# Kernel tuning notes

Hardware: AMD Instinct MI355X
Metric: run time of the kernel (lower is better)

## Reference

```python
import jax, jax.numpy as jnp
import numpy as np

N_DR, N_P, N_DIS = 8000, 20000, 5000
N_MF, N_BP, N_CC, N_PATH = 3000, 8000, 2000, 2392
H, B = 128, 65536
F_FINGER, F_SEQ, F_DIS = 1024, 400, 512
EPS = 1e-5


def _gcn(e, xs, ndst, W, b):
    # DGL GraphConv(norm='none', in==out): sum-aggregate src feats, then linear, then ReLU
    agg = jax.ops.segment_sum(xs[e[0]], e[1], num_segments=ndst)
    return jax.nn.relu(agg @ W + b)


def _sage(e, xs, xd, Wp, bp, Ws, Wn, b):
    # DGL SAGEConv(aggregator_type='pool'): max over relu(fc_pool(src)) + fc_self(dst), then ReLU
    h = jax.nn.relu(xs @ Wp + bp)
    agg = jax.ops.segment_max(h[e[0]], e[1], num_segments=xd.shape[0])
    agg = jnp.where(jnp.isfinite(agg), agg, 0.0)  # zero-in-degree dst -> 0 (DGL convention)
    return jax.nn.relu(xd @ Ws + agg @ Wn + b)


def _bn_relu(x, g, b):
    # BatchNorm1d in training mode (batch stats, biased var) + ReLU
    m = x.mean(0)
    v = x.var(0)
    return jax.nn.relu(g * (x - m) * jax.lax.rsqrt(v + EPS) + b)


def setup_inputs():
    key = jax.random.key(0)
    ks = iter(jax.random.split(key, 80))
    def nrm(shape, s=0.05):
        return jax.random.normal(next(ks), shape, dtype=jnp.float32) * s
    def edges(E, ns, nd):
        k1, k2 = jax.random.split(next(ks))
        return jnp.stack([jax.random.randint(k1, (E,), 0, ns, dtype=jnp.int32),
                          jax.random.randint(k2, (E,), 0, nd, dtype=jnp.int32)])
    inp = {}
    inp["x_dr"] = jax.random.randint(next(ks), (B, 1), 0, N_DR, dtype=jnp.int32)
    inp["x_p"] = jax.random.randint(next(ks), (B, 1), 0, N_P, dtype=jnp.int32)
    inp["finger_feats"] = nrm((N_DR, F_FINGER), 1.0)
    inp["seq_feats"] = nrm((N_P, F_SEQ), 1.0)
    inp["disease_feat"] = nrm((N_DIS, F_DIS), 1.0)
    inp["MF_feat"] = jnp.eye(N_MF, dtype=jnp.float32)   # identity feats, as in source
    inp["BP_feat"] = jnp.eye(N_BP, dtype=jnp.float32)
    inp["CC_feat"] = jnp.eye(N_CC, dtype=jnp.float32)
    inp["Pathway_feat"] = jnp.eye(N_PATH, dtype=jnp.float32)
    inp["e_dtdr"] = edges(100000, N_DIS, N_DR)
    inp["e_dmdr"] = edges(100000, N_DIS, N_DR)
    inp["e_dp"] = edges(200000, N_DIS, N_P)
    inp["e_drtd"] = edges(100000, N_DR, N_DIS)
    inp["e_drmd"] = edges(100000, N_DR, N_DIS)
    inp["e_pd"] = edges(200000, N_P, N_DIS)
    inp["e_ddi"] = edges(300000, N_DR, N_DR)
    inp["e_ppi"] = edges(600000, N_P, N_P)
    inp["e_mf_sim"] = edges(100000, N_MF, N_MF)
    inp["e_bp_sim"] = edges(300000, N_BP, N_BP)
    inp["e_cc_sim"] = edges(60000, N_CC, N_CC)
    inp["e_mf2p"] = edges(200000, N_MF, N_P)
    inp["e_bp2p"] = edges(400000, N_BP, N_P)
    inp["e_cc2p"] = edges(100000, N_CC, N_P)
    inp["e_path2p"] = edges(100000, N_PATH, N_P)
    inp["W_dr_emb"] = nrm((F_FINGER, H)); inp["b_dr_emb"] = jnp.zeros((H,), jnp.float32)
    inp["W_p_emb"] = nrm((F_SEQ, H)); inp["b_p_emb"] = jnp.zeros((H,), jnp.float32)
    inp["W_d_emb"] = nrm((F_DIS, H)); inp["b_d_emb"] = jnp.zeros((H,), jnp.float32)
    inp["W_mf_emb"] = nrm((N_MF, H)); inp["b_mf_emb"] = jnp.zeros((H,), jnp.float32)
    inp["W_bp_emb"] = nrm((N_BP, H)); inp["b_bp_emb"] = jnp.zeros((H,), jnp.float32)
    inp["W_cc_emb"] = nrm((N_CC, H)); inp["b_cc_emb"] = jnp.zeros((H,), jnp.float32)
    inp["W_path_emb"] = nrm((N_PATH, H)); inp["b_path_emb"] = jnp.zeros((H,), jnp.float32)
    inp["W_gcn"] = nrm((7, H, H)); inp["b_gcn"] = jnp.zeros((7, H), jnp.float32)
    inp["Wp_sage"] = nrm((8, H, H)); inp["bp_sage"] = jnp.zeros((8, H), jnp.float32)
    inp["Ws_sage"] = nrm((8, H, H)); inp["Wn_sage"] = nrm((8, H, H))
    inp["b_sage"] = jnp.zeros((8, H), jnp.float32)
    inp["W1"] = nrm((7 * H, 2 * H)); inp["b1"] = jnp.zeros((2 * H,), jnp.float32)
    inp["g1"] = jnp.ones((2 * H,), jnp.float32); inp["be1"] = jnp.zeros((2 * H,), jnp.float32)
    inp["W2"] = nrm((2 * H, H)); inp["b2"] = jnp.zeros((H,), jnp.float32)
    inp["g2"] = jnp.ones((H,), jnp.float32); inp["be2"] = jnp.zeros((H,), jnp.float32)
    inp["W3"] = nrm((H, 64)); inp["b3"] = jnp.zeros((64,), jnp.float32)
    inp["g3"] = jnp.ones((64,), jnp.float32); inp["be3"] = jnp.zeros((64,), jnp.float32)
    inp["Wo"] = nrm((64, 1)); inp["bo"] = jnp.zeros((1,), jnp.float32)
    return inp


def reference(x_dr, x_p, e_dtdr, e_dmdr, e_dp, e_drtd, e_drmd, e_pd, e_ddi, e_ppi,
              e_mf_sim, e_bp_sim, e_cc_sim, e_mf2p, e_bp2p, e_cc2p, e_path2p,
              finger_feats, seq_feats, disease_feat, MF_feat, BP_feat, CC_feat, Pathway_feat,
              W_dr_emb, b_dr_emb, W_p_emb, b_p_emb, W_d_emb, b_d_emb,
              W_mf_emb, b_mf_emb, W_bp_emb, b_bp_emb, W_cc_emb, b_cc_emb, W_path_emb, b_path_emb,
              W_gcn, b_gcn, Wp_sage, bp_sage, Ws_sage, Wn_sage, b_sage,
              W1, b1, g1, be1, W2, b2, g2, be2, W3, b3, g3, be3, Wo, bo):
    relu = jax.nn.relu
    # node-type input embeddings (Linear + ReLU)
    h_dr0 = relu(finger_feats @ W_dr_emb + b_dr_emb)
    h_p0 = relu(seq_feats @ W_p_emb + b_p_emb)
    h_d = relu(disease_feat @ W_d_emb + b_d_emb)
    h_mf = relu(MF_feat @ W_mf_emb + b_mf_emb)
    h_bp = relu(BP_feat @ W_bp_emb + b_bp_emb)
    h_cc = relu(CC_feat @ W_cc_emb + b_cc_emb)
    h_path = relu(Pathway_feat @ W_path_emb + b_path_emb)
    # GO similarity GCNs with residual
    mf = _gcn(e_mf_sim, h_mf, N_MF, W_gcn[0], b_gcn[0]) + h_mf
    bp = _gcn(e_bp_sim, h_bp, N_BP, W_gcn[1], b_gcn[1]) + h_bp
    cc = _gcn(e_cc_sim, h_cc, N_CC, W_gcn[2], b_gcn[2]) + h_cc
    # GO->protein and pathway->protein (HeteroGraphConv, sum aggregate)
    h_p_go = (_gcn(e_mf2p, mf, N_P, W_gcn[3], b_gcn[3])
              + _gcn(e_bp2p, bp, N_P, W_gcn[4], b_gcn[4])
              + _gcn(e_cc2p, cc, N_P, W_gcn[5], b_gcn[5]))
    h_p_path = _gcn(e_path2p, h_path, N_P, W_gcn[6], b_gcn[6])
    # heterogeneous SAGE layer over my_G (weights shared across the two applications)
    def S(i):
        return (Wp_sage[i], bp_sage[i], Ws_sage[i], Wn_sage[i], b_sage[i])
    def hetero(hdr, hp, hd):
        dr = (_sage(e_dtdr, hd, hdr, *S(0)) + _sage(e_dmdr, hd, hdr, *S(1))
              + _sage(e_ddi, hdr, hdr, *S(6)))
        p = _sage(e_dp, hd, hp, *S(2)) + _sage(e_ppi, hp, hp, *S(7))
        d = (_sage(e_drtd, hdr, hd, *S(3)) + _sage(e_drmd, hdr, hd, *S(4))
             + _sage(e_pd, hp, hd, *S(5)))
        return dr, p, d
    dr1, p1, d1 = hetero(h_dr0, h_p0, h_d)
    dr2, p2, _ = hetero(dr1, p1, d1)
    dr_new = jnp.concatenate([h_dr0, dr1, dr2], axis=1)                 # [N_DR, 3H]
    p_new = jnp.concatenate([h_p0, p1, p2, h_p_go + h_p_path], axis=1)  # [N_P, 4H]
    h = jnp.concatenate([dr_new[x_dr[:, 0]], p_new[x_p[:, 0]]], axis=1)  # [B, 7H]
    h = _bn_relu(h @ W1 + b1, g1, be1)
    h = _bn_relu(h @ W2 + b2, g2, be2)
    h = _bn_relu(h @ W3 + b3, g3, be3)
    return jax.nn.sigmoid(h @ Wo + bo)
```

## Files before the change

kernel.cpp:

```cpp
#include <hip/hip_runtime.h>

#define NCSR 15
#define MAXP 6
#define MAXT 8
#define NPT 21
#define NWT 37

typedef __attribute__((ext_vector_type(8))) short bfrag;
typedef __attribute__((ext_vector_type(4))) float ffrag;

__device__ __forceinline__ float b2f(unsigned short s) {
  return __uint_as_float(((unsigned int)s) << 16);
}
__device__ __forceinline__ unsigned short f2b(float f) {
  unsigned int u = __float_as_uint(f);
  u = (u + 0x7FFFu + ((u >> 16) & 1u)) >> 16;
  return (unsigned short)u;
}
__device__ __forceinline__ float ldf(const void* p, size_t i, int bf) {
  if (bf) return b2f(((const unsigned short*)p)[i]);
  return ((const float*)p)[i];
}
__device__ __forceinline__ int4 ld8(const void* p, size_t i, int bf) {
  if (bf) return *(const int4*)((const unsigned short*)p + i);
  const float* pf = (const float*)p + i;
  float4 f0 = *(const float4*)pf;
  float4 f1 = *(const float4*)(pf + 4);
  int4 v;
  v.x = (int)((unsigned)f2b(f0.x) | ((unsigned)f2b(f0.y) << 16));
  v.y = (int)((unsigned)f2b(f0.z) | ((unsigned)f2b(f0.w) << 16));
  v.z = (int)((unsigned)f2b(f1.x) | ((unsigned)f2b(f1.y) << 16));
  v.w = (int)((unsigned)f2b(f1.z) | ((unsigned)f2b(f1.w) << 16));
  return v;
}

struct CsrDesc {
  const int* src; const int* dst; int E; int n_dst;
  int* rowptr; unsigned short* csrc; int* slot; int pad;
};
struct CsrArgs { CsrDesc d[NCSR]; };

struct PTask { const void* src; float* dst; int n; int pad; };
struct PArgs { PTask t[NPT]; };

struct WTask { const void* src; unsigned short* dst; int K; int N; int eoff; int pad; };
struct WArgs { WTask t[NWT]; };

struct MPass { const unsigned short* A; const unsigned short* W; const float* bias; int lda; int ldw; int flags; };
struct MTask {
  MPass p[MAXP];
  const unsigned short* R; unsigned short* C;
  int npass, n, K, ldc, relu, pad;
};
struct MArgs { MTask t[MAXT]; };

struct GTask { const int* rowptr; const unsigned short* csrc; const unsigned short* X; unsigned short* out; int n_dst; int ldx; int mode; int pad; };
struct GArgs { GTask t[MAXT]; };

struct ETask { const void* A; const unsigned short* W; const float* bias; unsigned short* C; int n, K, ldc, pad; };
struct EArgs { ETask t[3]; };

struct BTask { const void* w; const float* b; unsigned short* out; int n; int pad[3]; };
struct BArgs { BTask t[4]; };

__global__ void k_flag(const unsigned int* probe, int* flag) {
  if (threadIdx.x == 0) *flag = (probe[0] == 0x3F800000u) ? 0 : 1;
}

__global__ void k_cv_params(PArgs args, const int* __restrict__ flagp) {
  const int bf = *flagp;
  const PTask T = args.t[blockIdx.y];
  for (int i = blockIdx.x * blockDim.x + threadIdx.x; i < T.n; i += gridDim.x * blockDim.x)
    T.dst[i] = ldf(T.src, (size_t)i, bf);
}

__global__ void k_cv_wt(WArgs args, const int* __restrict__ flagp) {
  const int bf = *flagp;
  const WTask T = args.t[blockIdx.y];
  const int total = T.K * T.N;
  const size_t eoff = (size_t)T.eoff;
  for (int i = blockIdx.x * blockDim.x + threadIdx.x; i < total; i += gridDim.x * blockDim.x) {
    int n = i / T.K, k = i - n * T.K;
    T.dst[i] = f2b(ldf(T.src, eoff + (size_t)k * T.N + n, bf));
  }
}

__global__ void k_biasrelu_multi(BArgs args, const int* __restrict__ flagp) {
  const int bf = *flagp;
  const BTask T = args.t[blockIdx.y];
  const int n8 = T.n >> 3;
  for (int i = blockIdx.x * blockDim.x + threadIdx.x; i < n8; i += gridDim.x * blockDim.x) {
    int base = i << 3;
    int4 v = ld8(T.w, (size_t)base, bf);
    const unsigned short* pv = (const unsigned short*)&v;
    const int cb = base & 127;
    unsigned short o[8];
#pragma unroll
    for (int j = 0; j < 8; ++j) {
      float f = b2f(pv[j]) + T.b[cb + j];
      o[j] = f2b(f > 0.f ? f : 0.f);
    }
    *(int4*)(T.out + base) = *(const int4*)o;
  }
}

__global__ void k_csr_count(CsrArgs args) {
  const CsrDesc cd = args.d[blockIdx.y];
  for (int e = blockIdx.x * blockDim.x + threadIdx.x; e < cd.E; e += gridDim.x * blockDim.x)
    cd.slot[e] = atomicAdd(&cd.rowptr[cd.dst[e] + 1], 1);
}

__global__ void k_csr_scan(CsrArgs args) {
  const CsrDesc cd = args.d[blockIdx.x];
  const int n = cd.n_dst + 1;
  const int t = threadIdx.x;
  const int lane = t & 63, w = t >> 6;
  __shared__ int wsum[16];
  int carry = 0;
  for (int base = 0; base < n; base += 1024) {
    int i = base + t;
    int v = (i < n) ? cd.rowptr[i] : 0;
    for (int off = 1; off < 64; off <<= 1) {
      int u = __shfl_up(v, off, 64);
      if (lane >= off) v += u;
    }
    if (lane == 63) wsum[w] = v;
    __syncthreads();
    if (w == 0) {
      int s = (lane < 16) ? wsum[lane] : 0;
      for (int off = 1; off < 16; off <<= 1) {
        int u = __shfl_up(s, off, 64);
        if (lane >= off) s += u;
      }
      if (lane < 16) wsum[lane] = s;
    }
    __syncthreads();
    int nv = v + carry + (w > 0 ? wsum[w - 1] : 0);
    if (i < n) cd.rowptr[i] = nv;
    carry += wsum[15];
    __syncthreads();
  }
}

__global__ void k_csr_fill(CsrArgs args) {
  const CsrDesc cd = args.d[blockIdx.y];
  for (int e = blockIdx.x * blockDim.x + threadIdx.x; e < cd.E; e += gridDim.x * blockDim.x) {
    int d = cd.dst[e];
    cd.csrc[cd.rowptr[d] + cd.slot[e]] = (unsigned short)cd.src[e];
  }
}

__global__ void k_gather_multi(GArgs args) {
  const GTask T = args.t[blockIdx.y];
  int w = (blockIdx.x * blockDim.x + threadIdx.x) >> 6;
  if (w >= T.n_dst) return;
  int lane = threadIdx.x & 63;
  int beg = T.rowptr[w], end = T.rowptr[w + 1];
  float a0 = 0.f, a1 = 0.f;
  int j = beg;
  if (T.mode == 0) {
    for (; j + 3 < end; j += 4) {
      unsigned int u0 = ((const unsigned int*)(T.X + (size_t)T.csrc[j] * T.ldx))[lane];
      unsigned int u1 = ((const unsigned int*)(T.X + (size_t)T.csrc[j + 1] * T.ldx))[lane];
      unsigned int u2 = ((const unsigned int*)(T.X + (size_t)T.csrc[j + 2] * T.ldx))[lane];
      unsigned int u3 = ((const unsigned int*)(T.X + (size_t)T.csrc[j + 3] * T.ldx))[lane];
      a0 += __uint_as_float(u0 << 16) + __uint_as_float(u1 << 16)
          + __uint_as_float(u2 << 16) + __uint_as_float(u3 << 16);
      a1 += __uint_as_float(u0 & 0xFFFF0000u) + __uint_as_float(u1 & 0xFFFF0000u)
          + __uint_as_float(u2 & 0xFFFF0000u) + __uint_as_float(u3 & 0xFFFF0000u);
    }
    for (; j < end; ++j) {
      unsigned int u0 = ((const unsigned int*)(T.X + (size_t)T.csrc[j] * T.ldx))[lane];
      a0 += __uint_as_float(u0 << 16);
      a1 += __uint_as_float(u0 & 0xFFFF0000u);
    }
  } else {
    for (; j + 3 < end; j += 4) {
      unsigned int u0 = ((const unsigned int*)(T.X + (size_t)T.csrc[j] * T.ldx))[lane];
      unsigned int u1 = ((const unsigned int*)(T.X + (size_t)T.csrc[j + 1] * T.ldx))[lane];
      unsigned int u2 = ((const unsigned int*)(T.X + (size_t)T.csrc[j + 2] * T.ldx))[lane];
      unsigned int u3 = ((const unsigned int*)(T.X + (size_t)T.csrc[j + 3] * T.ldx))[lane];
      a0 = fmaxf(fmaxf(a0, fmaxf(__uint_as_float(u0 << 16), __uint_as_float(u1 << 16))),
                 fmaxf(__uint_as_float(u2 << 16), __uint_as_float(u3 << 16)));
      a1 = fmaxf(fmaxf(a1, fmaxf(__uint_as_float(u0 & 0xFFFF0000u), __uint_as_float(u1 & 0xFFFF0000u))),
                 fmaxf(__uint_as_float(u2 & 0xFFFF0000u), __uint_as_float(u3 & 0xFFFF0000u)));
    }
    for (; j < end; ++j) {
      unsigned int u0 = ((const unsigned int*)(T.X + (size_t)T.csrc[j] * T.ldx))[lane];
      a0 = fmaxf(a0, __uint_as_float(u0 << 16));
      a1 = fmaxf(a1, __uint_as_float(u0 & 0xFFFF0000u));
    }
  }
  unsigned int* po = (unsigned int*)(T.out + (size_t)w * 128);
  po[lane] = (unsigned int)f2b(a0) | ((unsigned int)f2b(a1) << 16);
}

__launch_bounds__(256)
__global__ void k_mg(MArgs args) {
  const MTask* T = &args.t[blockIdx.y];
  const int n = T->n;
  const int row0 = blockIdx.x * 64;
  if (row0 >= n) return;
  __shared__ __align__(16) unsigned short As[64][72];
  __shared__ __align__(16) unsigned short Ws[128][72];
  const int t = threadIdx.x;
  const int wave = t >> 6, lane = t & 63;
  const int m16 = lane & 15, kq = lane >> 4;
  const int K = T->K;
  ffrag acc[4][2], accO[4][2];
#pragma unroll
  for (int i = 0; i < 4; ++i)
#pragma unroll
    for (int j = 0; j < 2; ++j) { acc[i][j] = (ffrag)0.f; accO[i][j] = (ffrag)0.f; }
  const int colbase = wave * 32;
  for (int ip = 0; ip < T->npass; ++ip) {
    const unsigned short* Ap = T->p[ip].A;
    const unsigned short* Wp = T->p[ip].W;
    const int lda = T->p[ip].lda, ldw = T->p[ip].ldw;
    for (int k0 = 0; k0 < K; k0 += 64) {
      __syncthreads();
#pragma unroll
      for (int e = t; e < 512; e += 256) {
        int r = e >> 3, c = e & 7;
        int row = row0 + r;
        int4 v = {0, 0, 0, 0};
        if (row < n) v = *(const int4*)(Ap + (size_t)row * lda + k0 + c * 8);
        *(int4*)&As[r][c * 8] = v;
      }
#pragma unroll
      for (int e = t; e < 1024; e += 256) {
        int nn = e >> 3, c = e & 7;
        *(int4*)&Ws[nn][c * 8] = *(const int4*)(Wp + (size_t)nn * ldw + k0 + c * 8);
      }
      __syncthreads();
#pragma unroll
      for (int kk = 0; kk < 64; kk += 32) {
        bfrag b0 = *(const bfrag*)&Ws[colbase + m16][kk + kq * 8];
        bfrag b1 = *(const bfrag*)&Ws[colbase + 16 + m16][kk + kq * 8];
#pragma unroll
        for (int rb = 0; rb < 4; ++rb) {
          bfrag a = *(const bfrag*)&As[rb * 16 + m16][kk + kq * 8];
          acc[rb][0] = __builtin_amdgcn_mfma_f32_16x16x32_bf16(a, b0, acc[rb][0], 0, 0, 0);
          acc[rb][1] = __builtin_amdgcn_mfma_f32_16x16x32_bf16(a, b1, acc[rb][1], 0, 0, 0);
        }
      }
    }
    if (T->p[ip].flags & 1) {
      const float* bias = T->p[ip].bias;
      float bv0 = bias ? bias[colbase + m16] : 0.f;
      float bv1 = bias ? bias[colbase + 16 + m16] : 0.f;
#pragma unroll
      for (int rb = 0; rb < 4; ++rb)
#pragma unroll
        for (int cb = 0; cb < 2; ++cb) {
          float bv = cb ? bv1 : bv0;
#pragma unroll
          for (int r = 0; r < 4; ++r) {
            float v = acc[rb][cb][r] + bv;
            if (T->relu) v = v > 0.f ? v : 0.f;
            accO[rb][cb][r] += v;
          }
          acc[rb][cb] = (ffrag)0.f;
        }
    }
  }
  const int ldc = T->ldc;
#pragma unroll
  for (int rb = 0; rb < 4; ++rb)
#pragma unroll
    for (int cb = 0; cb < 2; ++cb) {
      int col = colbase + cb * 16 + m16;
#pragma unroll
      for (int r = 0; r < 4; ++r) {
        int row = row0 + rb * 16 + kq * 4 + r;
        if (row < n) {
          float v = accO[rb][cb][r];
          if (T->R) v += b2f(T->R[(size_t)row * ldc + col]);
          T->C[(size_t)row * ldc + col] = f2b(v);
        }
      }
    }
}

__launch_bounds__(256)
__global__ void k_embed_multi(EArgs args, const int* __restrict__ flagp) {
  const ETask T = args.t[blockIdx.y];
  const int n = T.n;
  const int row0 = blockIdx.x * 32;
  if (row0 >= n) return;
  const int bf = *flagp;
  __shared__ __align__(16) unsigned short As[32][72];
  __shared__ __align__(16) unsigned short Ws[128][72];
  const int t = threadIdx.x;
  const int wave = t >> 6, lane = t & 63;
  const int m16 = lane & 15, kq = lane >> 4;
  const int K = T.K;
  ffrag acc[2][2];
#pragma unroll
  for (int i = 0; i < 2; ++i)
#pragma unroll
    for (int j = 0; j < 2; ++j) acc[i][j] = (ffrag)0.f;
  const int colbase = wave * 32;
  for (int k0 = 0; k0 < K; k0 += 64) {
    __syncthreads();
    {
      int r = t >> 3, c = t & 7;
      int row = row0 + r, k = k0 + c * 8;
      int4 v = {0, 0, 0, 0};
      if (row < n && k < K) v = ld8(T.A, (size_t)row * K + k, bf);
      *(int4*)&As[r][c * 8] = v;
    }
#pragma unroll
    for (int e = t; e < 1024; e += 256) {
      int nn = e >> 3, c = e & 7;
      int4 v = {0, 0, 0, 0};
      if (k0 + c * 8 < K) v = *(const int4*)(T.W + (size_t)nn * K + k0 + c * 8);
      *(int4*)&Ws[nn][c * 8] = v;
    }
    __syncthreads();
#pragma unroll
    for (int kk = 0; kk < 64; kk += 32) {
      bfrag a0 = *(const bfrag*)&As[m16][kk + kq * 8];
      bfrag a1 = *(const bfrag*)&As[16 + m16][kk + kq * 8];
      bfrag b0 = *(const bfrag*)&Ws[colbase + m16][kk + kq * 8];
      bfrag b1 = *(const bfrag*)&Ws[colbase + 16 + m16][kk + kq * 8];
      acc[0][0] = __builtin_amdgcn_mfma_f32_16x16x32_bf16(a0, b0, acc[0][0], 0, 0, 0);
      acc[0][1] = __builtin_amdgcn_mfma_f32_16x16x32_bf16(a0, b1, acc[0][1], 0, 0, 0);
      acc[1][0] = __builtin_amdgcn_mfma_f32_16x16x32_bf16(a1, b0, acc[1][0], 0, 0, 0);
      acc[1][1] = __builtin_amdgcn_mfma_f32_16x16x32_bf16(a1, b1, acc[1][1], 0, 0, 0);
    }
  }
#pragma unroll
  for (int rb = 0; rb < 2; ++rb)
#pragma unroll
    for (int cb = 0; cb < 2; ++cb) {
      int col = colbase + cb * 16 + m16;
      float bv = T.bias[col];
#pragma unroll
      for (int r = 0; r < 4; ++r) {
        int row = row0 + rb * 16 + kq * 4 + r;
        if (row < n) {
          float v = acc[rb][cb][r] + bv;
          T.C[(size_t)row * T.ldc + col] = f2b(v > 0.f ? v : 0.f);
        }
      }
    }
}

template<int NC>
__launch_bounds__(256)
__global__ void k_gemm_bn(const unsigned short* __restrict__ A, const unsigned short* __restrict__ W,
                          const float* __restrict__ bias, const float* __restrict__ ss,
                          unsigned short* __restrict__ C, double* __restrict__ st, int n, int K) {
  constexpr int CB = NC / 64;
  __shared__ __align__(16) unsigned short As[64][72];
  __shared__ __align__(16) unsigned short Ws[NC][72];
  const int t = threadIdx.x;
  const int wave = t >> 6, lane = t & 63;
  const int m16 = lane & 15, kq = lane >> 4;
  const int row0 = blockIdx.x * 64;
  if (row0 >= n) return;
  ffrag acc[4][CB];
#pragma unroll
  for (int i = 0; i < 4; ++i)
#pragma unroll
    for (int j = 0; j < CB; ++j) acc[i][j] = (ffrag)0.f;
  const int colbase = wave * 16 * CB;
  for (int k0 = 0; k0 < K; k0 += 64) {
    __syncthreads();
#pragma unroll
    for (int e = t; e < 512; e += 256) {
      int r = e >> 3, c = e & 7;
      int row = row0 + r, k = k0 + c * 8;
      int4 v = {0, 0, 0, 0};
      if (row < n) {
        int4 a8 = *(const int4*)(A + (size_t)row * K + k);
        const unsigned short* pa = (const unsigned short*)&a8;
        unsigned short o[8];
#pragma unroll
        for (int j = 0; j < 8; ++j) {
          float val = fmaf(b2f(pa[j]), ss[k + j], ss[K + k + j]);
          o[j] = f2b(val > 0.f ? val : 0.f);
        }
        v = *(const int4*)o;
      }
      *(int4*)&As[r][c * 8] = v;
    }
#pragma unroll
    for (int e = t; e < NC * 8; e += 256) {
      int nn = e >> 3, c = e & 7;
      *(int4*)&Ws[nn][c * 8] = *(const int4*)(W + (size_t)nn * K + k0 + c * 8);
    }
    __syncthreads();
#pragma unroll
    for (int kk = 0; kk < 64; kk += 32) {
#pragma unroll
      for (int cb = 0; cb < CB; ++cb) {
        bfrag b = *(const bfrag*)&Ws[colbase + cb * 16 + m16][kk + kq * 8];
#pragma unroll
        for (int rb = 0; rb < 4; ++rb) {
          bfrag a = *(const bfrag*)&As[rb * 16 + m16][kk + kq * 8];
          acc[rb][cb] = __builtin_amdgcn_mfma_f32_16x16x32_bf16(a, b, acc[rb][cb], 0, 0, 0);
        }
      }
    }
  }
#pragma unroll
  for (int cb = 0; cb < CB; ++cb) {
    int col = colbase + cb * 16 + m16;
    float bv = bias[col];
    float cs = 0.f, cq = 0.f;
#pragma unroll
    for (int rb = 0; rb < 4; ++rb) {
#pragma unroll
      for (int r = 0; r < 4; ++r) {
        int row = row0 + rb * 16 + kq * 4 + r;
        if (row < n) {
          float v = acc[rb][cb][r] + bv;
          C[(size_t)row * NC + col] = f2b(v);
          cs += v; cq += v * v;
        }
      }
    }
    cs += __shfl_xor(cs, 16); cs += __shfl_xor(cs, 32);
    cq += __shfl_xor(cq, 16); cq += __shfl_xor(cq, 32);
    if (kq == 0) {
      atomicAdd(&st[col], (double)cs);
      atomicAdd(&st[NC + col], (double)cq);
    }
  }
}

__global__ void k_hstat(const int* __restrict__ xdr, const int* __restrict__ xp,
                        const unsigned short* __restrict__ Udr, const unsigned short* __restrict__ Up,
                        double* __restrict__ st, int B) {
  __shared__ double sS[4][256];
  __shared__ double sQ[4][256];
  const int t = threadIdx.x;
  const int lane = t & 63, w = t >> 6;
  const int c4 = lane * 4;
  double s0 = 0, s1 = 0, s2 = 0, s3 = 0, q0 = 0, q1 = 0, q2 = 0, q3 = 0;
  const int NW = gridDim.x * 4;
  for (int r = blockIdx.x * 4 + w; r < B; r += NW) {
    int i = xdr[r], j = xp[r];
    uint2 a = *(const uint2*)(Udr + (size_t)i * 256 + c4);
    uint2 b = *(const uint2*)(Up + (size_t)j * 256 + c4);
    float v0 = b2f((unsigned short)a.x) + b2f((unsigned short)b.x);
    float v1 = b2f((unsigned short)(a.x >> 16)) + b2f((unsigned short)(b.x >> 16));
    float v2 = b2f((unsigned short)a.y) + b2f((unsigned short)b.y);
    float v3 = b2f((unsigned short)(a.y >> 16)) + b2f((unsigned short)(b.y >> 16));
    s0 += v0; s1 += v1; s2 += v2; s3 += v3;
    q0 += (double)v0 * (double)v0; q1 += (double)v1 * (double)v1;
    q2 += (double)v2 * (double)v2; q3 += (double)v3 * (double)v3;
  }
  sS[w][c4] = s0; sS[w][c4 + 1] = s1; sS[w][c4 + 2] = s2; sS[w][c4 + 3] = s3;
  sQ[w][c4] = q0; sQ[w][c4 + 1] = q1; sQ[w][c4 + 2] = q2; sQ[w][c4 + 3] = q3;
  __syncthreads();
  double ts = sS[0][t] + sS[1][t] + sS[2][t] + sS[3][t];
  double tq = sQ[0][t] + sQ[1][t] + sQ[2][t] + sQ[3][t];
  atomicAdd(&st[t], ts);
  atomicAdd(&st[256 + t], tq);
}

__launch_bounds__(256)
__global__ void k_gemm_bn1(const int* __restrict__ xdr, const int* __restrict__ xp,
                           const unsigned short* __restrict__ Udr, const unsigned short* __restrict__ Up,
                           const unsigned short* __restrict__ W, const float* __restrict__ bias,
                           const float* __restrict__ ss, unsigned short* __restrict__ Co,
                           double* __restrict__ st, int n) {
  __shared__ __align__(16) unsigned short As[64][72];
  __shared__ __align__(16) unsigned short Ws[128][72];
  __shared__ int gi[64], gj[64];
  const int t = threadIdx.x;
  const int wave = t >> 6, lane = t & 63;
  const int m16 = lane & 15, kq = lane >> 4;
  const int row0 = blockIdx.x * 64;
  if (row0 >= n) return;
  if (t < 64) {
    int row = row0 + t; if (row >= n) row = n - 1;
    gi[t] = xdr[row]; gj[t] = xp[row];
  }
  ffrag acc[4][2];
#pragma unroll
  for (int i = 0; i < 4; ++i)
#pragma unroll
    for (int j = 0; j < 2; ++j) acc[i][j] = (ffrag)0.f;
  const int colbase = wave * 32;
  __syncthreads();
  for (int k0 = 0; k0 < 256; k0 += 64) {
    __syncthreads();
#pragma unroll
    for (int e = t; e < 512; e += 256) {
      int r = e >> 3, seg = e & 7;
      int k = k0 + seg * 8;
      int4 a = *(const int4*)(Udr + (size_t)gi[r] * 256 + k);
      int4 b = *(const int4*)(Up + (size_t)gj[r] * 256 + k);
      const unsigned short* pa = (const unsigned short*)&a;
      const unsigned short* pb = (const unsigned short*)&b;
      unsigned short o[8];
#pragma unroll
      for (int jj = 0; jj < 8; ++jj) {
        float v = b2f(pa[jj]) + b2f(pb[jj]);
        v = fmaf(v, ss[k + jj], ss[256 + k + jj]);
        o[jj] = f2b(v > 0.f ? v : 0.f);
      }
      *(int4*)&As[r][seg * 8] = *(const int4*)o;
    }
#pragma unroll
    for (int e = t; e < 1024; e += 256) {
      int nn = e >> 3, c = e & 7;
      *(int4*)&Ws[nn][c * 8] = *(const int4*)(W + (size_t)nn * 256 + k0 + c * 8);
    }
    __syncthreads();
#pragma unroll
    for (int kk = 0; kk < 64; kk += 32) {
      bfrag b0 = *(const bfrag*)&Ws[colbase + m16][kk + kq * 8];
      bfrag b1 = *(const bfrag*)&Ws[colbase + 16 + m16][kk + kq * 8];
#pragma unroll
      for (int rb = 0; rb < 4; ++rb) {
        bfrag a = *(const bfrag*)&As[rb * 16 + m16][kk + kq * 8];
        acc[rb][0] = __builtin_amdgcn_mfma_f32_16x16x32_bf16(a, b0, acc[rb][0], 0, 0, 0);
        acc[rb][1] = __builtin_amdgcn_mfma_f32_16x16x32_bf16(a, b1, acc[rb][1], 0, 0, 0);
      }
    }
  }
#pragma unroll
  for (int cb = 0; cb < 2; ++cb) {
    int col = colbase + cb * 16 + m16;
    float bv = bias[col];
    float cs = 0.f, cq = 0.f;
#pragma unroll
    for (int rb = 0; rb < 4; ++rb) {
#pragma unroll
      for (int r = 0; r < 4; ++r) {
        int row = row0 + rb * 16 + kq * 4 + r;
        if (row < n) {
          float v = acc[rb][cb][r] + bv;
          Co[(size_t)row * 128 + col] = f2b(v);
          cs += v; cq += v * v;
        }
      }
    }
    cs += __shfl_xor(cs, 16); cs += __shfl_xor(cs, 32);
    cq += __shfl_xor(cq, 16); cq += __shfl_xor(cq, 32);
    if (kq == 0) {
      atomicAdd(&st[col], (double)cs);
      atomicAdd(&st[128 + col], (double)cq);
    }
  }
}

__global__ void k_bnfin(const double* __restrict__ st, int B, int C,
                        const float* __restrict__ g, const float* __restrict__ be,
                        float* __restrict__ ss) {
  int c = threadIdx.x;
  if (c < C) {
    double m = st[c] / B;
    double v = st[C + c] / B - m * m;
    if (v < 0) v = 0;
    float sc = (float)((double)g[c] / sqrt(v + 1e-5));
    ss[c] = sc;
    ss[C + c] = be[c] - (float)m * sc;
  }
}

__global__ void k_final(const unsigned short* __restrict__ Z3, const float* __restrict__ ss3,
                        const float* __restrict__ Wo, const float* __restrict__ bo,
                        void* __restrict__ out, int B, const int* __restrict__ flagp) {
  __shared__ float w[64], sc[64], sh[64];
  if (threadIdx.x < 64) {
    w[threadIdx.x] = Wo[threadIdx.x];
    sc[threadIdx.x] = ss3[threadIdx.x];
    sh[threadIdx.x] = ss3[64 + threadIdx.x];
  }
  __syncthreads();
  const int bf = *flagp;
  const float bb = bo[0];
  for (int r = blockIdx.x * blockDim.x + threadIdx.x; r < B; r += gridDim.x * blockDim.x) {
    const unsigned short* z = &Z3[(size_t)r * 64];
    float acc = bb;
#pragma unroll
    for (int k = 0; k < 64; ++k) {
      float y = fmaf(b2f(z[k]), sc[k], sh[k]);
      y = y > 0.f ? y : 0.f;
      acc = fmaf(y, w[k], acc);
    }
    float sv = 1.f / (1.f + expf(-acc));
    if (bf) ((unsigned short*)out)[r] = f2b(sv);
    else ((float*)out)[r] = sv;
  }
}

extern "C" void kernel_launch(void* const* d_in, const int* in_sizes, int n_in,
                              void* d_out, int out_size, void* d_ws, size_t ws_size,
                              hipStream_t stream) {
  enum { N_DR = 8000, N_P = 20000, N_DIS = 5000, N_MF = 3000, N_BP = 8000,
         N_CC = 2000, N_PATH = 2392 };
  if (n_in < 59) return;
  const int B = in_sizes[0];
  const int* x_dr = (const int*)d_in[0];
  const int* x_p  = (const int*)d_in[1];

  char* base = (char*)d_ws;
  size_t off = 0;
  auto alloc = [&](size_t bytes) -> void* {
    void* p = base + off;
    off += (bytes + 255) & ~(size_t)255;
    return p;
  };
  int*    flagp = (int*)alloc(256);
  double* st1 = (double*)alloc(896 * sizeof(double));
  double* st2 = st1 + 512; double* st3 = st2 + 256;
  float*  ss1 = (float*)alloc(896 * sizeof(float));
  float*  ss2 = ss1 + 512; float* ss3 = ss2 + 256;
  float*  pbuf = (float*)alloc(6000 * sizeof(float));
  unsigned short* wbf = (unsigned short*)alloc(1100000 * 2);
  unsigned short* DR  = (unsigned short*)alloc((size_t)N_DR * 384 * 2);
  unsigned short* P   = (unsigned short*)alloc((size_t)N_P * 512 * 2);
  unsigned short* h_d = (unsigned short*)alloc((size_t)N_DIS * 128 * 2);
  unsigned short* d1b = (unsigned short*)alloc((size_t)N_DIS * 128 * 2);
  unsigned short* z1  = (unsigned short*)alloc((size_t)B * 256 * 2);
  char* arena = (char*)alloc(44u * 1024 * 1024);
  if (off > ws_size) return;

  unsigned short* ar = (unsigned short*)arena;
  unsigned short* A_hmf  = ar;
  unsigned short* A_hbp  = A_hmf + (size_t)N_MF * 128;
  unsigned short* A_hcc  = A_hbp + (size_t)N_BP * 128;
  unsigned short* A_hpath= A_hcc + (size_t)N_CC * 128;
  unsigned short* A_gomf = A_hpath + (size_t)N_PATH * 128;
  unsigned short* A_gobp = A_gomf + (size_t)N_MF * 128;
  unsigned short* A_gocc = A_gobp + (size_t)N_BP * 128;
  unsigned short* ag17 = A_gocc + (size_t)N_CC * 128;
  unsigned short* ag18 = ag17 + (size_t)N_MF * 128;
  unsigned short* ag19 = ag18 + (size_t)N_BP * 128;
  unsigned short* ag20 = ag19 + (size_t)N_CC * 128;
  unsigned short* ag21 = ag20 + (size_t)N_P * 128;
  unsigned short* ag22 = ag21 + (size_t)N_P * 128;
  unsigned short* ag23 = ag22 + (size_t)N_P * 128;
  unsigned short* pl0 = ar;
  unsigned short* pl1 = pl0 + (size_t)N_DIS * 128;
  unsigned short* pl2 = pl1 + (size_t)N_DIS * 128;
  unsigned short* pl3 = pl2 + (size_t)N_DIS * 128;
  unsigned short* pl4 = pl3 + (size_t)N_DR * 128;
  unsigned short* pl5 = pl4 + (size_t)N_DR * 128;
  unsigned short* pl6 = pl5 + (size_t)N_P * 128;
  unsigned short* pl7 = pl6 + (size_t)N_DR * 128;
  unsigned short* ag9  = pl7 + (size_t)N_P * 128;
  unsigned short* ag10 = ag9 + (size_t)N_DR * 128;
  unsigned short* ag11 = ag10 + (size_t)N_DR * 128;
  unsigned short* ag12 = ag11 + (size_t)N_P * 128;
  unsigned short* ag13 = ag12 + (size_t)N_DIS * 128;
  unsigned short* ag14 = ag13 + (size_t)N_DIS * 128;
  unsigned short* ag15 = ag14 + (size_t)N_DIS * 128;
  unsigned short* ag16 = ag15 + (size_t)N_DR * 128;
  unsigned short* U_dr = ar;
  unsigned short* U_p  = U_dr + (size_t)N_DR * 256;
  unsigned short* z2 = U_p + (size_t)N_P * 256;
  unsigned short* z3 = z1;
  int* slot_arena = (int*)arena;

  k_flag<<<1, 64, 0, stream>>>((const unsigned int*)d_in[5], flagp);

  float* pp[59] = {};
  {
    PArgs pa;
    const int pidx[NPT] = {25,27,29,31,33,35,37,39,41,44,46,47,48,50,51,52,54,55,56,57,58};
    size_t poff = 0;
    for (int l = 0; l < NPT; ++l) {
      int i = pidx[l];
      pa.t[l].src = d_in[i]; pa.t[l].dst = pbuf + poff; pa.t[l].n = in_sizes[i]; pa.t[l].pad = 0;
      pp[i] = pbuf + poff;
      poff += in_sizes[i];
    }
    k_cv_params<<<dim3(4, NPT), 256, 0, stream>>>(pa, flagp);
  }

  unsigned short *Wdr_t, *Wpe_t, *Wde_t, *Wg_t, *Wps_t, *Wss_t, *Wns_t, *W1_t, *W2_t, *W3_t;
  {
    WArgs wa;
    int l = 0; size_t woff = 0;
    auto add = [&](int inIdx, int eoff, int K, int N) -> unsigned short* {
      unsigned short* dst = wbf + woff;
      wa.t[l].src = d_in[inIdx]; wa.t[l].dst = dst; wa.t[l].K = K; wa.t[l].N = N;
      wa.t[l].eoff = eoff; wa.t[l].pad = 0;
      ++l; woff += (size_t)K * N;
      return dst;
    };
    Wdr_t = add(24, 0, 1024, 128);
    Wpe_t = add(26, 0, 400, 128);
    Wde_t = add(28, 0, 512, 128);
    Wg_t = wbf + woff;
    for (int j = 0; j < 7; ++j) add(38, j * 16384, 128, 128);
    Wps_t = wbf + woff;
    for (int j = 0; j < 8; ++j) add(40, j * 16384, 128, 128);
    Wss_t = wbf + woff;
    for (int j = 0; j < 8; ++j) add(42, j * 16384, 128, 128);
    Wns_t = wbf + woff;
    for (int j = 0; j < 8; ++j) add(43, j * 16384, 128, 128);
    W1_t = add(45, 0, 896, 256);
    W2_t = add(49, 0, 256, 128);
    W3_t = add(53, 0, 128, 64);
    k_cv_wt<<<dim3(32, NWT), 256, 0, stream>>>(wa, flagp);
  }

  const int list_ei[NCSR] = {9, 10, 11, 12, 13, 14, 15, 16, 17, 18, 19, 20, 21, 22, 23};
  const int list_nd[NCSR] = {N_DR, N_DR, N_P, N_DIS, N_DIS, N_DIS, N_DR, N_P,
                             N_MF, N_BP, N_CC, N_P, N_P, N_P, N_P};
  int* rp[24]; unsigned short* cs[24];
  CsrArgs csra;
  {
    int* ip = (int*)z1;
    int* rp0 = ip;
    for (int l = 0; l < NCSR; ++l) { csra.d[l].rowptr = ip; rp[list_ei[l]] = ip; ip += list_nd[l] + 1; }
    size_t rp_total = (size_t)(ip - rp0);
    unsigned short* up = (unsigned short*)ip;
    size_t slotoff = 0;
    for (int l = 0; l < NCSR; ++l) {
      int ei = list_ei[l];
      int E = in_sizes[ei] / 2;
      csra.d[l].src = (const int*)d_in[ei];
      csra.d[l].dst = (const int*)d_in[ei] + E;
      csra.d[l].E = E;
      csra.d[l].n_dst = list_nd[l];
      csra.d[l].csrc = up; cs[ei] = up;
      csra.d[l].slot = slot_arena + slotoff;
      csra.d[l].pad = 0;
      up += E;
      slotoff += E;
    }
    hipMemsetAsync(rp0, 0, rp_total * sizeof(int), stream);
  }
  k_csr_count<<<dim3(96, NCSR), 256, 0, stream>>>(csra);
  k_csr_scan<<<NCSR, 1024, 0, stream>>>(csra);
  k_csr_fill<<<dim3(96, NCSR), 256, 0, stream>>>(csra);

  hipMemsetAsync(st1, 0, 896 * sizeof(double), stream);

  {
    EArgs ea;
    ea.t[0] = {d_in[2], Wdr_t, pp[25], DR, N_DR, 1024, 384, 0};
    ea.t[1] = {d_in[3], Wpe_t, pp[27], P, N_P, 400, 512, 0};
    ea.t[2] = {d_in[4], Wde_t, pp[29], h_d, N_DIS, 512, 128, 0};
    k_embed_multi<<<dim3((N_P + 31) / 32, 3), 256, 0, stream>>>(ea, flagp);
  }
  {
    BArgs ba;
    ba.t[0] = {d_in[30], pp[31], A_hmf, N_MF * 128, {}};
    ba.t[1] = {d_in[32], pp[33], A_hbp, N_BP * 128, {}};
    ba.t[2] = {d_in[34], pp[35], A_hcc, N_CC * 128, {}};
    ba.t[3] = {d_in[36], pp[37], A_hpath, N_PATH * 128, {}};
    k_biasrelu_multi<<<dim3(128, 4), 256, 0, stream>>>(ba, flagp);
  }

  auto mkpass = [](MTask& T, int i, const unsigned short* A, int lda, const unsigned short* W,
                   int ldw, const float* bias, int end) {
    T.p[i].A = A; T.p[i].lda = lda; T.p[i].W = W; T.p[i].ldw = ldw;
    T.p[i].bias = bias; T.p[i].flags = end;
  };
  const float* bg = pp[39];
  const float* bp_s = pp[41];
  const float* b_s = pp[44];

  {
    GArgs ga;
    ga.t[0] = {rp[17], cs[17], A_hmf, ag17, N_MF, 128, 0, 0};
    ga.t[1] = {rp[18], cs[18], A_hbp, ag18, N_BP, 128, 0, 0};
    ga.t[2] = {rp[19], cs[19], A_hcc, ag19, N_CC, 128, 0, 0};
    k_gather_multi<<<dim3((N_BP + 3) / 4, 3), 256, 0, stream>>>(ga);
  }
  {
    MArgs ma;
    for (int i = 0; i < 3; ++i) {
      MTask& T = ma.t[i];
      const unsigned short* aggp = (i == 0) ? ag17 : (i == 1) ? ag18 : ag19;
      const unsigned short* Rp = (i == 0) ? A_hmf : (i == 1) ? A_hbp : A_hcc;
      unsigned short* Cp = (i == 0) ? A_gomf : (i == 1) ? A_gobp : A_gocc;
      int n = (i == 0) ? N_MF : (i == 1) ? N_BP : N_CC;
      mkpass(T, 0, aggp, 128, Wg_t + (size_t)i * 16384, 128, bg + i * 128, 1);
      T.npass = 1; T.n = n; T.K = 128; T.R = Rp; T.C = Cp; T.ldc = 128; T.relu = 1;
    }
    k_mg<<<dim3((N_BP + 63) / 64, 3), 256, 0, stream>>>(ma);
  }
  {
    GArgs ga;
    ga.t[0] = {rp[20], cs[20], A_gomf, ag20, N_P, 128, 0, 0};
    ga.t[1] = {rp[21], cs[21], A_gobp, ag21, N_P, 128, 0, 0};
    ga.t[2] = {rp[22], cs[22], A_gocc, ag22, N_P, 128, 0, 0};
    ga.t[3] = {rp[23], cs[23], A_hpath, ag23, N_P, 128, 0, 0};
    k_gather_multi<<<dim3((N_P + 3) / 4, 4), 256, 0, stream>>>(ga);
  }
  {
    MArgs ma;
    MTask& T = ma.t[0];
    mkpass(T, 0, ag20, 128, Wg_t + 3 * 16384, 128, bg + 3 * 128, 1);
    mkpass(T, 1, ag21, 128, Wg_t + 4 * 16384, 128, bg + 4 * 128, 1);
    mkpass(T, 2, ag22, 128, Wg_t + 5 * 16384, 128, bg + 5 * 128, 1);
    mkpass(T, 3, ag23, 128, Wg_t + 6 * 16384, 128, bg + 6 * 128, 1);
    T.npass = 4; T.n = N_P; T.K = 128; T.R = nullptr; T.C = P + 384; T.ldc = 512; T.relu = 1;
    k_mg<<<dim3((N_P + 63) / 64, 1), 256, 0, stream>>>(ma);
  }

  {
    MArgs ma;
    const unsigned short* xs[8] = {h_d, h_d, h_d, DR, DR, P, DR, P};
    const int lda[8] = {128, 128, 128, 384, 384, 512, 384, 512};
    const int nn[8] = {N_DIS, N_DIS, N_DIS, N_DR, N_DR, N_P, N_DR, N_P};
    unsigned short* plo[8] = {pl0, pl1, pl2, pl3, pl4, pl5, pl6, pl7};
    for (int i = 0; i < 8; ++i) {
      MTask& T = ma.t[i];
      mkpass(T, 0, xs[i], lda[i], Wps_t + (size_t)i * 16384, 128, bp_s + i * 128, 1);
      T.npass = 1; T.n = nn[i]; T.K = 128; T.R = nullptr; T.C = plo[i]; T.ldc = 128; T.relu = 1;
    }
    k_mg<<<dim3((N_P + 63) / 64, 8), 256, 0, stream>>>(ma);
  }
  {
    GArgs ga;
    ga.t[0] = {rp[9],  cs[9],  pl0, ag9,  N_DR, 128, 1, 0};
    ga.t[1] = {rp[10], cs[10], pl1, ag10, N_DR, 128, 1, 0};
    ga.t[2] = {rp[11], cs[11], pl2, ag11, N_P, 128, 1, 0};
    ga.t[3] = {rp[12], cs[12], pl3, ag12, N_DIS, 128, 1, 0};
    ga.t[4] = {rp[13], cs[13], pl4, ag13, N_DIS, 128, 1, 0};
    ga.t[5] = {rp[14], cs[14], pl5, ag14, N_DIS, 128, 1, 0};
    ga.t[6] = {rp[15], cs[15], pl6, ag15, N_DR, 128, 1, 0};
    ga.t[7] = {rp[16], cs[16], pl7, ag16, N_P, 128, 1, 0};
    k_gather_multi<<<dim3((N_P + 3) / 4, 8), 256, 0, stream>>>(ga);
  }
  {
    MArgs ma;
    {
      MTask& T = ma.t[0];
      mkpass(T, 0, DR, 384, Wss_t + (size_t)0 * 16384, 128, nullptr, 0);
      mkpass(T, 1, ag9, 128, Wns_t + (size_t)0 * 16384, 128, b_s + 0 * 128, 1);
      mkpass(T, 2, DR, 384, Wss_t + (size_t)1 * 16384, 128, nullptr, 0);
      mkpass(T, 3, ag10, 128, Wns_t + (size_t)1 * 16384, 128, b_s + 1 * 128, 1);
      mkpass(T, 4, DR, 384, Wss_t + (size_t)6 * 16384, 128, nullptr, 0);
      mkpass(T, 5, ag15, 128, Wns_t + (size_t)6 * 16384, 128, b_s + 6 * 128, 1);
      T.npass = 6; T.n = N_DR; T.K = 128; T.R = nullptr; T.C = DR + 128; T.ldc = 384; T.relu = 1;
    }
    {
      MTask& T = ma.t[1];
      mkpass(T, 0, P, 512, Wss_t + (size_t)2 * 16384, 128, nullptr, 0);
      mkpass(T, 1, ag11, 128, Wns_t + (size_t)2 * 16384, 128, b_s + 2 * 128, 1);
      mkpass(T, 2, P, 512, Wss_t + (size_t)7 * 16384, 128, nullptr, 0);
      mkpass(T, 3, ag16, 128, Wns_t + (size_t)7 * 16384, 128, b_s + 7 * 128, 1);
      T.npass = 4; T.n = N_P; T.K = 128; T.R = nullptr; T.C = P + 128; T.ldc = 512; T.relu = 1;
    }
    {
      MTask& T = ma.t[2];
      mkpass(T, 0, h_d, 128, Wss_t + (size_t)3 * 16384, 128, nullptr, 0);
      mkpass(T, 1, ag12, 128, Wns_t + (size_t)3 * 16384, 128, b_s + 3 * 128, 1);
      mkpass(T, 2, h_d, 128, Wss_t + (size_t)4 * 16384, 128, nullptr, 0);
      mkpass(T, 3, ag13, 128, Wns_t + (size_t)4 * 16384, 128, b_s + 4 * 128, 1);
      mkpass(T, 4, h_d, 128, Wss_t + (size_t)5 * 16384, 128, nullptr, 0);
      mkpass(T, 5, ag14, 128, Wns_t + (size_t)5 * 16384, 128, b_s + 5 * 128, 1);
      T.npass = 6; T.n = N_DIS; T.K = 128; T.R = nullptr; T.C = d1b; T.ldc = 128; T.relu = 1;
    }
    k_mg<<<dim3((N_P + 63) / 64, 3), 256, 0, stream>>>(ma);
  }

  {
    MArgs ma;
    const unsigned short* xs[5] = {d1b, d1b, d1b, DR + 128, P + 128};
    const int lda[5] = {128, 128, 128, 384, 512};
    const int nn[5] = {N_DIS, N_DIS, N_DIS, N_DR, N_P};
    unsigned short* plo[5] = {pl0, pl1, pl2, pl6, pl7};
    const int si[5] = {0, 1, 2, 6, 7};
    for (int i = 0; i < 5; ++i) {
      MTask& T = ma.t[i];
      mkpass(T, 0, xs[i], lda[i], Wps_t + (size_t)si[i] * 16384, 128, bp_s + si[i] * 128, 1);
      T.npass = 1; T.n = nn[i]; T.K = 128; T.R = nullptr; T.C = plo[i]; T.ldc = 128; T.relu = 1;
    }
    k_mg<<<dim3((N_P + 63) / 64, 5), 256, 0, stream>>>(ma);
  }
  {
    GArgs ga;
    ga.t[0] = {rp[9],  cs[9],  pl0, ag9,  N_DR, 128, 1, 0};
    ga.t[1] = {rp[10], cs[10], pl1, ag10, N_DR, 128, 1, 0};
    ga.t[2] = {rp[11], cs[11], pl2, ag11, N_P, 128, 1, 0};
    ga.t[3] = {rp[15], cs[15], pl6, ag15, N_DR, 128, 1, 0};
    ga.t[4] = {rp[16], cs[16], pl7, ag16, N_P, 128, 1, 0};
    k_gather_multi<<<dim3((N_P + 3) / 4, 5), 256, 0, stream>>>(ga);
  }
  {
    MArgs ma;
    {
      MTask& T = ma.t[0];
      mkpass(T, 0, DR + 128, 384, Wss_t + (size_t)0 * 16384, 128, nullptr, 0);
      mkpass(T, 1, ag9, 128, Wns_t + (size_t)0 * 16384, 128, b_s + 0 * 128, 1);
      mkpass(T, 2, DR + 128, 384, Wss_t + (size_t)1 * 16384, 128, nullptr, 0);
      mkpass(T, 3, ag10, 128, Wns_t + (size_t)1 * 16384, 128, b_s + 1 * 128, 1);
      mkpass(T, 4, DR + 128, 384, Wss_t + (size_t)6 * 16384, 128, nullptr, 0);
      mkpass(T, 5, ag15, 128, Wns_t + (size_t)6 * 16384, 128, b_s + 6 * 128, 1);
      T.npass = 6; T.n = N_DR; T.K = 128; T.R = nullptr; T.C = DR + 256; T.ldc = 384; T.relu = 1;
    }
    {
      MTask& T = ma.t[1];
      mkpass(T, 0, P + 128, 512, Wss_t + (size_t)2 * 16384, 128, nullptr, 0);
      mkpass(T, 1, ag11, 128, Wns_t + (size_t)2 * 16384, 128, b_s + 2 * 128, 1);
      mkpass(T, 2, P + 128, 512, Wss_t + (size_t)7 * 16384, 128, nullptr, 0);
      mkpass(T, 3, ag16, 128, Wns_t + (size_t)7 * 16384, 128, b_s + 7 * 128, 1);
      T.npass = 4; T.n = N_P; T.K = 128; T.R = nullptr; T.C = P + 256; T.ldc = 512; T.relu = 1;
    }
    k_mg<<<dim3((N_P + 63) / 64, 2), 256, 0, stream>>>(ma);
  }

  {
    MArgs ma;
    for (int half = 0; half < 2; ++half) {
      {
        MTask& T = ma.t[half];
        mkpass(T, 0, DR, 384, W1_t + (size_t)(half * 128) * 896, 896, pp[46] + half * 128, 1);
        T.npass = 1; T.n = N_DR; T.K = 384; T.R = nullptr;
        T.C = U_dr + half * 128; T.ldc = 256; T.relu = 0;
      }
      {
        MTask& T = ma.t[2 + half];
        mkpass(T, 0, P, 512, W1_t + (size_t)(half * 128) * 896 + 384, 896, nullptr, 1);
        T.npass = 1; T.n = N_P; T.K = 512; T.R = nullptr;
        T.C = U_p + half * 128; T.ldc = 256; T.relu = 0;
      }
    }
    k_mg<<<dim3((N_P + 63) / 64, 4), 256, 0, stream>>>(ma);
  }

  k_hstat<<<256, 256, 0, stream>>>(x_dr, x_p, U_dr, U_p, st1, B);
  k_bnfin<<<1, 256, 0, stream>>>(st1, B, 256, pp[47], pp[48], ss1);

  k_gemm_bn1<<<(B + 63) / 64, 256, 0, stream>>>(x_dr, x_p, U_dr, U_p, W2_t, pp[50], ss1, z2, st2, B);
  k_bnfin<<<1, 128, 0, stream>>>(st2, B, 128, pp[51], pp[52], ss2);

  k_gemm_bn<64><<<(B + 63) / 64, 256, 0, stream>>>(z2, W3_t, pp[54], ss2, z3, st3, B, 128);
  k_bnfin<<<1, 64, 0, stream>>>(st3, B, 64, pp[55], pp[56], ss3);

  k_final<<<256, 256, 0, stream>>>(z3, ss3, pp[57], pp[58], d_out, B, flagp);
}
```

Baseline: 1.215 ms.

## Merge independent stages into fused multi-task launches with compact block offsets

Merges the parameter and weight conversion into one launch, and CSR counting, embedding and bias-ReLU into another. Every grouped GEMM or gather launch now indexes tasks through prefix offsets, so blocks for small tasks are no longer padded to the largest task's size. Independent work from different pipeline stages is reordered to share a launch, for example CSR fill with the pool GEMMs and GO gathers with SAGE layer-2 pool GEMMs. This cuts launch count and idle blocks, but requires relocating scratch buffers and adds an early-return guard if the arena overflows.

```diff
diff --git a/kernel.cpp b/kernel.cpp
--- a/kernel.cpp
+++ b/kernel.cpp
@@ -3,6 +3,7 @@
 #define NCSR 15
 #define MAXP 6
 #define MAXT 8
+#define MAXG 12
 #define NPT 21
 #define NWT 37
 
@@ -52,10 +53,8 @@
   const unsigned short* R; unsigned short* C;
   int npass, n, K, ldc, relu, pad;
 };
-struct MArgs { MTask t[MAXT]; };
 
 struct GTask { const int* rowptr; const unsigned short* csrc; const unsigned short* X; unsigned short* out; int n_dst; int ldx; int mode; int pad; };
-struct GArgs { GTask t[MAXT]; };
 
 struct ETask { const void* A; const unsigned short* W; const float* bias; unsigned short* C; int n, K, ldc, pad; };
 struct EArgs { ETask t[3]; };
@@ -63,33 +62,32 @@
 struct BTask { const void* w; const float* b; unsigned short* out; int n; int pad[3]; };
 struct BArgs { BTask t[4]; };
 
-__global__ void k_flag(const unsigned int* probe, int* flag) {
-  if (threadIdx.x == 0) *flag = (probe[0] == 0x3F800000u) ? 0 : 1;
-}
-
-__global__ void k_cv_params(PArgs args, const int* __restrict__ flagp) {
-  const int bf = *flagp;
-  const PTask T = args.t[blockIdx.y];
-  for (int i = blockIdx.x * blockDim.x + threadIdx.x; i < T.n; i += gridDim.x * blockDim.x)
-    T.dst[i] = ldf(T.src, (size_t)i, bf);
-}
-
-__global__ void k_cv_wt(WArgs args, const int* __restrict__ flagp) {
-  const int bf = *flagp;
-  const WTask T = args.t[blockIdx.y];
-  const int total = T.K * T.N;
-  const size_t eoff = (size_t)T.eoff;
-  for (int i = blockIdx.x * blockDim.x + threadIdx.x; i < total; i += gridDim.x * blockDim.x) {
-    int n = i / T.K, k = i - n * T.K;
-    T.dst[i] = f2b(ldf(T.src, eoff + (size_t)k * T.N + n, bf));
-  }
-}
-
-__global__ void k_biasrelu_multi(BArgs args, const int* __restrict__ flagp) {
-  const int bf = *flagp;
-  const BTask T = args.t[blockIdx.y];
+struct GSup { GTask t[MAXG]; int off[MAXG + 1]; int nt; };
+struct MSup { MTask t[MAXT]; int off[MAXT + 1]; int nt; };
+
+__device__ __forceinline__ int find_task(const int* off, int nt, int bx, int& lx) {
+  int t = 0;
+  while (t + 1 < nt && bx >= off[t + 1]) ++t;
+  lx = bx - off[t];
+  return t;
+}
+
+
+__device__ void count_body(const CsrDesc& cd, int lx) {
+  for (int e = lx * 256 + (int)threadIdx.x; e < cd.E; e += 96 * 256)
+    cd.slot[e] = atomicAdd(&cd.rowptr[cd.dst[e] + 1], 1);
+}
+
+__device__ void fill_body(const CsrDesc& cd, int lx) {
+  for (int e = lx * 256 + (int)threadIdx.x; e < cd.E; e += 96 * 256) {
+    int d = cd.dst[e];
+    cd.csrc[cd.rowptr[d] + cd.slot[e]] = (unsigned short)cd.src[e];
+  }
+}
+
+__device__ void bias_body(const BTask& T, int lx, int bf) {
   const int n8 = T.n >> 3;
-  for (int i = blockIdx.x * blockDim.x + threadIdx.x; i < n8; i += gridDim.x * blockDim.x) {
+  for (int i = lx * 256 + (int)threadIdx.x; i < n8; i += 128 * 256) {
     int base = i << 3;
     int4 v = ld8(T.w, (size_t)base, bf);
     const unsigned short* pv = (const unsigned short*)&v;
@@ -104,55 +102,8 @@
   }
 }
 
-__global__ void k_csr_count(CsrArgs args) {
-  const CsrDesc cd = args.d[blockIdx.y];
-  for (int e = blockIdx.x * blockDim.x + threadIdx.x; e < cd.E; e += gridDim.x * blockDim.x)
-    cd.slot[e] = atomicAdd(&cd.rowptr[cd.dst[e] + 1], 1);
-}
-
-__global__ void k_csr_scan(CsrArgs args) {
-  const CsrDesc cd = args.d[blockIdx.x];
-  const int n = cd.n_dst + 1;
-  const int t = threadIdx.x;
-  const int lane = t & 63, w = t >> 6;
-  __shared__ int wsum[16];
-  int carry = 0;
-  for (int base = 0; base < n; base += 1024) {
-    int i = base + t;
-    int v = (i < n) ? cd.rowptr[i] : 0;
-    for (int off = 1; off < 64; off <<= 1) {
-      int u = __shfl_up(v, off, 64);
-      if (lane >= off) v += u;
-    }
-    if (lane == 63) wsum[w] = v;
-    __syncthreads();
-    if (w == 0) {
-      int s = (lane < 16) ? wsum[lane] : 0;
-      for (int off = 1; off < 16; off <<= 1) {
-        int u = __shfl_up(s, off, 64);
-        if (lane >= off) s += u;
-      }
-      if (lane < 16) wsum[lane] = s;
-    }
-    __syncthreads();
-    int nv = v + carry + (w > 0 ? wsum[w - 1] : 0);
-    if (i < n) cd.rowptr[i] = nv;
-    carry += wsum[15];
-    __syncthreads();
-  }
-}
-
-__global__ void k_csr_fill(CsrArgs args) {
-  const CsrDesc cd = args.d[blockIdx.y];
-  for (int e = blockIdx.x * blockDim.x + threadIdx.x; e < cd.E; e += gridDim.x * blockDim.x) {
-    int d = cd.dst[e];
-    cd.csrc[cd.rowptr[d] + cd.slot[e]] = (unsigned short)cd.src[e];
-  }
-}
-
-__global__ void k_gather_multi(GArgs args) {
-  const GTask T = args.t[blockIdx.y];
-  int w = (blockIdx.x * blockDim.x + threadIdx.x) >> 6;
+__device__ void gather_body(const GTask& T, int lx) {
+  int w = lx * 4 + ((int)threadIdx.x >> 6);
   if (w >= T.n_dst) return;
   int lane = threadIdx.x & 63;
   int beg = T.rowptr[w], end = T.rowptr[w + 1];
@@ -195,11 +146,9 @@
   po[lane] = (unsigned int)f2b(a0) | ((unsigned int)f2b(a1) << 16);
 }
 
-__launch_bounds__(256)
-__global__ void k_mg(MArgs args) {
-  const MTask* T = &args.t[blockIdx.y];
+__device__ void mg_body(const MTask* T, int lx) {
   const int n = T->n;
-  const int row0 = blockIdx.x * 64;
+  const int row0 = lx * 64;
   if (row0 >= n) return;
   __shared__ __align__(16) unsigned short As[64][72];
   __shared__ __align__(16) unsigned short Ws[128][72];
@@ -282,13 +231,10 @@
     }
 }
 
-__launch_bounds__(256)
-__global__ void k_embed_multi(EArgs args, const int* __restrict__ flagp) {
-  const ETask T = args.t[blockIdx.y];
+__device__ void embed_body(const ETask& T, int lx, int bf) {
   const int n = T.n;
-  const int row0 = blockIdx.x * 32;
+  const int row0 = lx * 32;
   if (row0 >= n) return;
-  const int bf = *flagp;
   __shared__ __align__(16) unsigned short As[32][72];
   __shared__ __align__(16) unsigned short Ws[128][72];
   const int t = threadIdx.x;
@@ -345,6 +291,109 @@
         }
       }
     }
+}
+
+
+__global__ void k_flag(const unsigned int* probe, int* flag) {
+  if (threadIdx.x == 0) *flag = (probe[0] == 0x3F800000u) ? 0 : 1;
+}
+
+__launch_bounds__(256)
+__global__ void k_cv(PArgs pa, WArgs wa, const int* __restrict__ flagp) {
+  const int bf = *flagp;
+  int bx = blockIdx.x;
+  if (bx < NPT * 4) {
+    const PTask T = pa.t[bx >> 2];
+    for (int i = (bx & 3) * 256 + (int)threadIdx.x; i < T.n; i += 4 * 256)
+      T.dst[i] = ldf(T.src, (size_t)i, bf);
+  } else {
+    bx -= NPT * 4;
+    const WTask T = wa.t[bx >> 5];
+    const int lx = bx & 31;
+    const int total = T.K * T.N;
+    const size_t eoff = (size_t)T.eoff;
+    for (int i = lx * 256 + (int)threadIdx.x; i < total; i += 32 * 256) {
+      int n = i / T.K, k = i - n * T.K;
+      T.dst[i] = f2b(ldf(T.src, eoff + (size_t)k * T.N + n, bf));
+    }
+  }
+}
+
+__launch_bounds__(256)
+__global__ void k_prep(CsrArgs csr, EArgs ea, BArgs ba, const int* __restrict__ flagp) {
+  int bx = blockIdx.x;
+  if (bx < NCSR * 96) { count_body(csr.d[bx / 96], bx % 96); return; }
+  bx -= NCSR * 96;
+  if (bx < 1032) {
+    int t, lx;
+    if (bx < 250) { t = 0; lx = bx; }
+    else if (bx < 875) { t = 1; lx = bx - 250; }
+    else { t = 2; lx = bx - 875; }
+    embed_body(ea.t[t], lx, *flagp);
+    return;
+  }
+  bx -= 1032;
+  bias_body(ba.t[bx >> 7], bx & 127, *flagp);
+}
+
+__global__ void k_csr_scan(CsrArgs args) {
+  const CsrDesc cd = args.d[blockIdx.x];
+  const int n = cd.n_dst + 1;
+  const int t = threadIdx.x;
+  const int lane = t & 63, w = t >> 6;
+  __shared__ int wsum[16];
+  int carry = 0;
+  for (int base = 0; base < n; base += 1024) {
+    int i = base + t;
+    int v = (i < n) ? cd.rowptr[i] : 0;
+    for (int off = 1; off < 64; off <<= 1) {
+      int u = __shfl_up(v, off, 64);
+      if (lane >= off) v += u;
+    }
+    if (lane == 63) wsum[w] = v;
+    __syncthreads();
+    if (w == 0) {
+      int s = (lane < 16) ? wsum[lane] : 0;
+      for (int off = 1; off < 16; off <<= 1) {
+        int u = __shfl_up(s, off, 64);
+        if (lane >= off) s += u;
+      }
+      if (lane < 16) wsum[lane] = s;
+    }
+    __syncthreads();
+    int nv = v + carry + (w > 0 ? wsum[w - 1] : 0);
+    if (i < n) cd.rowptr[i] = nv;
+    carry += wsum[15];
+    __syncthreads();
+  }
+}
+
+__launch_bounds__(256)
+__global__ void k_fillmg(CsrArgs csr, MSup ms) {
+  int bx = blockIdx.x;
+  if (bx < NCSR * 96) { fill_body(csr.d[bx / 96], bx % 96); return; }
+  bx -= NCSR * 96;
+  int lx; int t = find_task(ms.off, ms.nt, bx, lx);
+  mg_body(&ms.t[t], lx);
+}
+
+__global__ void k_gsup(GSup gs) {
+  int lx; int t = find_task(gs.off, gs.nt, blockIdx.x, lx);
+  gather_body(gs.t[t], lx);
+}
+
+__launch_bounds__(256)
+__global__ void k_gm(GSup gs, MSup ms) {
+  int bx = blockIdx.x;
+  const int gtot = gs.off[gs.nt];
+  if (bx < gtot) {
+    int lx; int t = find_task(gs.off, gs.nt, bx, lx);
+    gather_body(gs.t[t], lx);
+    return;
+  }
+  bx -= gtot;
+  int lx; int t = find_task(ms.off, ms.nt, bx, lx);
+  mg_body(&ms.t[t], lx);
 }
 
 template<int NC>
@@ -633,38 +682,28 @@
   unsigned short* A_gocc = A_gobp + (size_t)N_BP * 128;
   unsigned short* ag17 = A_gocc + (size_t)N_CC * 128;
   unsigned short* ag18 = ag17 + (size_t)N_MF * 128;
-  unsigned short* ag19 = ag18 + (size_t)N_BP * 128;
-  unsigned short* ag20 = ag19 + (size_t)N_CC * 128;
-  unsigned short* ag21 = ag20 + (size_t)N_P * 128;
-  unsigned short* ag22 = ag21 + (size_t)N_P * 128;
-  unsigned short* ag23 = ag22 + (size_t)N_P * 128;
-  unsigned short* pl0 = ar;
-  unsigned short* pl1 = pl0 + (size_t)N_DIS * 128;
-  unsigned short* pl2 = pl1 + (size_t)N_DIS * 128;
-  unsigned short* pl3 = pl2 + (size_t)N_DIS * 128;
-  unsigned short* pl4 = pl3 + (size_t)N_DR * 128;
-  unsigned short* pl5 = pl4 + (size_t)N_DR * 128;
-  unsigned short* pl6 = pl5 + (size_t)N_P * 128;
-  unsigned short* pl7 = pl6 + (size_t)N_DR * 128;
-  unsigned short* ag9  = pl7 + (size_t)N_P * 128;
-  unsigned short* ag10 = ag9 + (size_t)N_DR * 128;
+  unsigned short* ag9  = ag18 + (size_t)N_BP * 128;
+  unsigned short* ag10 = ag9  + (size_t)N_DR * 128;
   unsigned short* ag11 = ag10 + (size_t)N_DR * 128;
   unsigned short* ag12 = ag11 + (size_t)N_P * 128;
   unsigned short* ag13 = ag12 + (size_t)N_DIS * 128;
   unsigned short* ag14 = ag13 + (size_t)N_DIS * 128;
   unsigned short* ag15 = ag14 + (size_t)N_DIS * 128;
   unsigned short* ag16 = ag15 + (size_t)N_DR * 128;
+  unsigned short* ag21 = ag16 + (size_t)N_P * 128;
+  unsigned short* ag22 = ag21 + (size_t)N_P * 128;
+  unsigned short* ag23 = ag22 + (size_t)N_P * 128;
   unsigned short* U_dr = ar;
   unsigned short* U_p  = U_dr + (size_t)N_DR * 256;
   unsigned short* z2 = U_p + (size_t)N_P * 256;
   unsigned short* z3 = z1;
-  int* slot_arena = (int*)arena;
+  int* slot_arena = (int*)(ar + (size_t)7168000);
 
   k_flag<<<1, 64, 0, stream>>>((const unsigned int*)d_in[5], flagp);
 
   float* pp[59] = {};
-  {
-    PArgs pa;
+  PArgs pa;
+  {
     const int pidx[NPT] = {25,27,29,31,33,35,37,39,41,44,46,47,48,50,51,52,54,55,56,57,58};
     size_t poff = 0;
     for (int l = 0; l < NPT; ++l) {
@@ -673,12 +712,10 @@
       pp[i] = pbuf + poff;
       poff += in_sizes[i];
     }
-    k_cv_params<<<dim3(4, NPT), 256, 0, stream>>>(pa, flagp);
-  }
-
+  }
   unsigned short *Wdr_t, *Wpe_t, *Wde_t, *Wg_t, *Wps_t, *Wss_t, *Wns_t, *W1_t, *W2_t, *W3_t;
-  {
-    WArgs wa;
+  WArgs wa;
+  {
     int l = 0; size_t woff = 0;
     auto add = [&](int inIdx, int eoff, int K, int N) -> unsigned short* {
       unsigned short* dst = wbf + woff;
@@ -701,14 +738,15 @@
     W1_t = add(45, 0, 896, 256);
     W2_t = add(49, 0, 256, 128);
     W3_t = add(53, 0, 128, 64);
-    k_cv_wt<<<dim3(32, NWT), 256, 0, stream>>>(wa, flagp);
-  }
+  }
+  k_cv<<<NPT * 4 + NWT * 32, 256, 0, stream>>>(pa, wa, flagp);
 
   const int list_ei[NCSR] = {9, 10, 11, 12, 13, 14, 15, 16, 17, 18, 19, 20, 21, 22, 23};
   const int list_nd[NCSR] = {N_DR, N_DR, N_P, N_DIS, N_DIS, N_DIS, N_DR, N_P,
                              N_MF, N_BP, N_CC, N_P, N_P, N_P, N_P};
   int* rp[24]; unsigned short* cs[24];
   CsrArgs csra;
+  unsigned short* csr_end;
   {
     int* ip = (int*)z1;
     int* rp0 = ip;
@@ -729,29 +767,23 @@
       up += E;
       slotoff += E;
     }
+    csr_end = up;
     hipMemsetAsync(rp0, 0, rp_total * sizeof(int), stream);
   }
-  k_csr_count<<<dim3(96, NCSR), 256, 0, stream>>>(csra);
-  k_csr_scan<<<NCSR, 1024, 0, stream>>>(csra);
-  k_csr_fill<<<dim3(96, NCSR), 256, 0, stream>>>(csra);
+  unsigned short* plb = (unsigned short*)(((uintptr_t)csr_end + 255) & ~(uintptr_t)255);
+  unsigned short* plz0 = plb;
+  unsigned short* plz1 = plz0 + (size_t)N_DIS * 128;
+  unsigned short* plz2 = plz1 + (size_t)N_DIS * 128;
+  unsigned short* plz3 = plz2 + (size_t)N_DIS * 128;
+  unsigned short* plz4 = plz3 + (size_t)N_DR * 128;
+  unsigned short* plz5 = plz4 + (size_t)N_DR * 128;
+  unsigned short* plz6 = plz5 + (size_t)N_P * 128;
+  unsigned short* plz7 = plz6 + (size_t)N_DR * 128;
+  unsigned short* ag19 = plz7 + (size_t)N_P * 128;
+  unsigned short* ag20 = ag19 + (size_t)N_CC * 128;
+  if ((ag20 + (size_t)N_P * 128) > (z1 + (size_t)B * 256)) return;
 
   hipMemsetAsync(st1, 0, 896 * sizeof(double), stream);
-
-  {
-    EArgs ea;
-    ea.t[0] = {d_in[2], Wdr_t, pp[25], DR, N_DR, 1024, 384, 0};
-    ea.t[1] = {d_in[3], Wpe_t, pp[27], P, N_P, 400, 512, 0};
-    ea.t[2] = {d_in[4], Wde_t, pp[29], h_d, N_DIS, 512, 128, 0};
-    k_embed_multi<<<dim3((N_P + 31) / 32, 3), 256, 0, stream>>>(ea, flagp);
-  }
-  {
-    BArgs ba;
-    ba.t[0] = {d_in[30], pp[31], A_hmf, N_MF * 128, {}};
-    ba.t[1] = {d_in[32], pp[33], A_hbp, N_BP * 128, {}};
-    ba.t[2] = {d_in[34], pp[35], A_hcc, N_CC * 128, {}};
-    ba.t[3] = {d_in[36], pp[37], A_hpath, N_PATH * 128, {}};
-    k_biasrelu_multi<<<dim3(128, 4), 256, 0, stream>>>(ba, flagp);
-  }
 
   auto mkpass = [](MTask& T, int i, const unsigned short* A, int lda, const unsigned short* W,
                    int ldw, const float* bias, int end) {
@@ -762,74 +794,81 @@
   const float* bp_s = pp[41];
   const float* b_s = pp[44];
 
-  {
-    GArgs ga;
-    ga.t[0] = {rp[17], cs[17], A_hmf, ag17, N_MF, 128, 0, 0};
-    ga.t[1] = {rp[18], cs[18], A_hbp, ag18, N_BP, 128, 0, 0};
-    ga.t[2] = {rp[19], cs[19], A_hcc, ag19, N_CC, 128, 0, 0};
-    k_gather_multi<<<dim3((N_BP + 3) / 4, 3), 256, 0, stream>>>(ga);
-  }
-  {
-    MArgs ma;
+  auto gadd = [](GSup& g, GTask t) {
+    if (g.nt == 0) g.off[0] = 0;
+    g.t[g.nt] = t;
+    g.off[g.nt + 1] = g.off[g.nt] + (t.n_dst + 3) / 4;
+    g.nt++;
+  };
+  auto madd = [](MSup& m, const MTask& t) {
+    if (m.nt == 0) m.off[0] = 0;
+    m.t[m.nt] = t;
+    m.off[m.nt + 1] = m.off[m.nt] + (t.n + 63) / 64;
+    m.nt++;
+  };
+
+  {
+    EArgs ea;
+    ea.t[0] = {d_in[2], Wdr_t, pp[25], DR, N_DR, 1024, 384, 0};
+    ea.t[1] = {d_in[3], Wpe_t, pp[27], P, N_P, 400, 512, 0};
+    ea.t[2] = {d_in[4], Wde_t, pp[29], h_d, N_DIS, 512, 128, 0};
+    BArgs ba;
+    ba.t[0] = {d_in[30], pp[31], A_hmf, N_MF * 128, {}};
+    ba.t[1] = {d_in[32], pp[33], A_hbp, N_BP * 128, {}};
+    ba.t[2] = {d_in[34], pp[35], A_hcc, N_CC * 128, {}};
+    ba.t[3] = {d_in[36], pp[37], A_hpath, N_PATH * 128, {}};
+    k_prep<<<NCSR * 96 + 1032 + 4 * 128, 256, 0, stream>>>(csra, ea, ba, flagp);
+  }
+
+  k_csr_scan<<<NCSR, 1024, 0, stream>>>(csra);
+
+  {
+    MSup ms; ms.nt = 0;
+    const unsigned short* xs[8] = {h_d, h_d, h_d, DR, DR, P, DR, P};
+    const int lda[8] = {128, 128, 128, 384, 384, 512, 384, 512};
+    const int nn[8] = {N_DIS, N_DIS, N_DIS, N_DR, N_DR, N_P, N_DR, N_P};
+    unsigned short* plo[8] = {plz0, plz1, plz2, plz3, plz4, plz5, plz6, plz7};
+    for (int i = 0; i < 8; ++i) {
+      MTask T;
+      mkpass(T, 0, xs[i], lda[i], Wps_t + (size_t)i * 16384, 128, bp_s + i * 128, 1);
+      T.npass = 1; T.n = nn[i]; T.K = 128; T.R = nullptr; T.C = plo[i]; T.ldc = 128; T.relu = 1;
+      madd(ms, T);
+    }
+    k_fillmg<<<NCSR * 96 + ms.off[ms.nt], 256, 0, stream>>>(csra, ms);
+  }
+
+  {
+    GSup gs; gs.nt = 0;
+    gadd(gs, {rp[17], cs[17], A_hmf, ag17, N_MF, 128, 0, 0});
+    gadd(gs, {rp[18], cs[18], A_hbp, ag18, N_BP, 128, 0, 0});
+    gadd(gs, {rp[19], cs[19], A_hcc, ag19, N_CC, 128, 0, 0});
+    gadd(gs, {rp[9],  cs[9],  plz0, ag9,  N_DR, 128, 1, 0});
+    gadd(gs, {rp[10], cs[10], plz1, ag10, N_DR, 128, 1, 0});
+    gadd(gs, {rp[11], cs[11], plz2, ag11, N_P, 128, 1, 0});
+    gadd(gs, {rp[12], cs[12], plz3, ag12, N_DIS, 128, 1, 0});
+    gadd(gs, {rp[13], cs[13], plz4, ag13, N_DIS, 128, 1, 0});
+    gadd(gs, {rp[14], cs[14], plz5, ag14, N_DIS, 128, 1, 0});
+    gadd(gs, {rp[15], cs[15], plz6, ag15, N_DR, 128, 1, 0});
+    gadd(gs, {rp[16], cs[16], plz7, ag16, N_P, 128, 1, 0});
+    k_gsup<<<gs.off[gs.nt], 256, 0, stream>>>(gs);
+  }
+
+  GSup g0; g0.nt = 0; g0.off[0] = 0;
+
+  {
+    MSup ms; ms.nt = 0;
     for (int i = 0; i < 3; ++i) {
-      MTask& T = ma.t[i];
+      MTask T;
       const unsigned short* aggp = (i == 0) ? ag17 : (i == 1) ? ag18 : ag19;
       const unsigned short* Rp = (i == 0) ? A_hmf : (i == 1) ? A_hbp : A_hcc;
       unsigned short* Cp = (i == 0) ? A_gomf : (i == 1) ? A_gobp : A_gocc;
       int n = (i == 0) ? N_MF : (i == 1) ? N_BP : N_CC;
       mkpass(T, 0, aggp, 128, Wg_t + (size_t)i * 16384, 128, bg + i * 128, 1);
       T.npass = 1; T.n = n; T.K = 128; T.R = Rp; T.C = Cp; T.ldc = 128; T.relu = 1;
-    }
-    k_mg<<<dim3((N_BP + 63) / 64, 3), 256, 0, stream>>>(ma);
-  }
-  {
-    GArgs ga;
-    ga.t[0] = {rp[20], cs[20], A_gomf, ag20, N_P, 128, 0, 0};
-    ga.t[1] = {rp[21], cs[21], A_gobp, ag21, N_P, 128, 0, 0};
-    ga.t[2] = {rp[22], cs[22], A_gocc, ag22, N_P, 128, 0, 0};
-    ga.t[3] = {rp[23], cs[23], A_hpath, ag23, N_P, 128, 0, 0};
-    k_gather_multi<<<dim3((N_P + 3) / 4, 4), 256, 0, stream>>>(ga);
-  }
-  {
-    MArgs ma;
-    MTask& T = ma.t[0];
-    mkpass(T, 0, ag20, 128, Wg_t + 3 * 16384, 128, bg + 3 * 128, 1);
-    mkpass(T, 1, ag21, 128, Wg_t + 4 * 16384, 128, bg + 4 * 128, 1);
-    mkpass(T, 2, ag22, 128, Wg_t + 5 * 16384, 128, bg + 5 * 128, 1);
-    mkpass(T, 3, ag23, 128, Wg_t + 6 * 16384, 128, bg + 6 * 128, 1);
-    T.npass = 4; T.n = N_P; T.K = 128; T.R = nullptr; T.C = P + 384; T.ldc = 512; T.relu = 1;
-    k_mg<<<dim3((N_P + 63) / 64, 1), 256, 0, stream>>>(ma);
-  }
-
-  {
-    MArgs ma;
-    const unsigned short* xs[8] = {h_d, h_d, h_d, DR, DR, P, DR, P};
-    const int lda[8] = {128, 128, 128, 384, 384, 512, 384, 512};
-    const int nn[8] = {N_DIS, N_DIS, N_DIS, N_DR, N_DR, N_P, N_DR, N_P};
-    unsigned short* plo[8] = {pl0, pl1, pl2, pl3, pl4, pl5, pl6, pl7};
-    for (int i = 0; i < 8; ++i) {
-      MTask& T = ma.t[i];
-      mkpass(T, 0, xs[i], lda[i], Wps_t + (size_t)i * 16384, 128, bp_s + i * 128, 1);
-      T.npass = 1; T.n = nn[i]; T.K = 128; T.R = nullptr; T.C = plo[i]; T.ldc = 128; T.relu = 1;
-    }
-    k_mg<<<dim3((N_P + 63) / 64, 8), 256, 0, stream>>>(ma);
-  }
-  {
-    GArgs ga;
-    ga.t[0] = {rp[9],  cs[9],  pl0, ag9,  N_DR, 128, 1, 0};
-    ga.t[1] = {rp[10], cs[10], pl1, ag10, N_DR, 128, 1, 0};
-    ga.t[2] = {rp[11], cs[11], pl2, ag11, N_P, 128, 1, 0};
-    ga.t[3] = {rp[12], cs[12], pl3, ag12, N_DIS, 128, 1, 0};
-    ga.t[4] = {rp[13], cs[13], pl4, ag13, N_DIS, 128, 1, 0};
-    ga.t[5] = {rp[14], cs[14], pl5, ag14, N_DIS, 128, 1, 0};
-    ga.t[6] = {rp[15], cs[15], pl6, ag15, N_DR, 128, 1, 0};
-    ga.t[7] = {rp[16], cs[16], pl7, ag16, N_P, 128, 1, 0};
-    k_gather_multi<<<dim3((N_P + 3) / 4, 8), 256, 0, stream>>>(ga);
-  }
-  {
-    MArgs ma;
+      madd(ms, T);
+    }
     {
-      MTask& T = ma.t[0];
+      MTask T;
       mkpass(T, 0, DR, 384, Wss_t + (size_t)0 * 16384, 128, nullptr, 0);
       mkpass(T, 1, ag9, 128, Wns_t + (size_t)0 * 16384, 128, b_s + 0 * 128, 1);
       mkpass(T, 2, DR, 384, Wss_t + (size_t)1 * 16384, 128, nullptr, 0);
@@ -837,17 +876,19 @@
       mkpass(T, 4, DR, 384, Wss_t + (size_t)6 * 16384, 128, nullptr, 0);
       mkpass(T, 5, ag15, 128, Wns_t + (size_t)6 * 16384, 128, b_s + 6 * 128, 1);
       T.npass = 6; T.n = N_DR; T.K = 128; T.R = nullptr; T.C = DR + 128; T.ldc = 384; T.relu = 1;
+      madd(ms, T);
     }
     {
-      MTask& T = ma.t[1];
+      MTask T;
       mkpass(T, 0, P, 512, Wss_t + (size_t)2 * 16384, 128, nullptr, 0);
       mkpass(T, 1, ag11, 128, Wns_t + (size_t)2 * 16384, 128, b_s + 2 * 128, 1);
       mkpass(T, 2, P, 512, Wss_t + (size_t)7 * 16384, 128, nullptr, 0);
       mkpass(T, 3, ag16, 128, Wns_t + (size_t)7 * 16384, 128, b_s + 7 * 128, 1);
       T.npass = 4; T.n = N_P; T.K = 128; T.R = nullptr; T.C = P + 128; T.ldc = 512; T.relu = 1;
+      madd(ms, T);
     }
     {
-      MTask& T = ma.t[2];
+      MTask T;
       mkpass(T, 0, h_d, 128, Wss_t + (size_t)3 * 16384, 128, nullptr, 0);
       mkpass(T, 1, ag12, 128, Wns_t + (size_t)3 * 16384, 128, b_s + 3 * 128, 1);
       mkpass(T, 2, h_d, 128, Wss_t + (size_t)4 * 16384, 128, nullptr, 0);
@@ -855,37 +896,54 @@
       mkpass(T, 4, h_d, 128, Wss_t + (size_t)5 * 16384, 128, nullptr, 0);
       mkpass(T, 5, ag14, 128, Wns_t + (size_t)5 * 16384, 128, b_s + 5 * 128, 1);
       T.npass = 6; T.n = N_DIS; T.K = 128; T.R = nullptr; T.C = d1b; T.ldc = 128; T.relu = 1;
-    }
-    k_mg<<<dim3((N_P + 63) / 64, 3), 256, 0, stream>>>(ma);
-  }
-
-  {
-    MArgs ma;
+      madd(ms, T);
+    }
+    k_gm<<<ms.off[ms.nt], 256, 0, stream>>>(g0, ms);
+  }
+
+  {
+    GSup gs; gs.nt = 0;
+    gadd(gs, {rp[20], cs[20], A_gomf, ag20, N_P, 128, 0, 0});
+    gadd(gs, {rp[21], cs[21], A_gobp, ag21, N_P, 128, 0, 0});
+    gadd(gs, {rp[22], cs[22], A_gocc, ag22, N_P, 128, 0, 0});
+    gadd(gs, {rp[23], cs[23], A_hpath, ag23, N_P, 128, 0, 0});
+    MSup ms; ms.nt = 0;
     const unsigned short* xs[5] = {d1b, d1b, d1b, DR + 128, P + 128};
     const int lda[5] = {128, 128, 128, 384, 512};
     const int nn[5] = {N_DIS, N_DIS, N_DIS, N_DR, N_P};
-    unsigned short* plo[5] = {pl0, pl1, pl2, pl6, pl7};
+    unsigned short* plo[5] = {plz0, plz1, plz2, plz6, plz7};
     const int si[5] = {0, 1, 2, 6, 7};
     for (int i = 0; i < 5; ++i) {
-      MTask& T = ma.t[i];
+      MTask T;
       mkpass(T, 0, xs[i], lda[i], Wps_t + (size_t)si[i] * 16384, 128, bp_s + si[i] * 128, 1);
       T.npass = 1; T.n = nn[i]; T.K = 128; T.R = nullptr; T.C = plo[i]; T.ldc = 128; T.relu = 1;
-    }
-    k_mg<<<dim3((N_P + 63) / 64, 5), 256, 0, stream>>>(ma);
-  }
-  {
-    GArgs ga;
-    ga.t[0] = {rp[9],  cs[9],  pl0, ag9,  N_DR, 128, 1, 0};
-    ga.t[1] = {rp[10], cs[10], pl1, ag10, N_DR, 128, 1, 0};
-    ga.t[2] = {rp[11], cs[11], pl2, ag11, N_P, 128, 1, 0};
-    ga.t[3] = {rp[15], cs[15], pl6, ag15, N_DR, 128, 1, 0};
-    ga.t[4] = {rp[16], cs[16], pl7, ag16, N_P, 128, 1, 0};
-    k_gather_multi<<<dim3((N_P + 3) / 4, 5), 256, 0, stream>>>(ga);
-  }
-  {
-    MArgs ma;
+      madd(ms, T);
+    }
+    k_gm<<<gs.off[gs.nt] + ms.off[ms.nt], 256, 0, stream>>>(gs, ms);
+  }
+
+  {
+    GSup gs; gs.nt = 0;
+    gadd(gs, {rp[9],  cs[9],  plz0, ag9,  N_DR, 128, 1, 0});
+    gadd(gs, {rp[10], cs[10], plz1, ag10, N_DR, 128, 1, 0});
+    gadd(gs, {rp[11], cs[11], plz2, ag11, N_P, 128, 1, 0});
+    gadd(gs, {rp[15], cs[15], plz6, ag15, N_DR, 128, 1, 0});
+    gadd(gs, {rp[16], cs[16], plz7, ag16, N_P, 128, 1, 0});
+    MSup ms; ms.nt = 0;
+    MTask T;
+    mkpass(T, 0, ag20, 128, Wg_t + 3 * 16384, 128, bg + 3 * 128, 1);
+    mkpass(T, 1, ag21, 128, Wg_t + 4 * 16384, 128, bg + 4 * 128, 1);
+    mkpass(T, 2, ag22, 128, Wg_t + 5 * 16384, 128, bg + 5 * 128, 1);
+    mkpass(T, 3, ag23, 128, Wg_t + 6 * 16384, 128, bg + 6 * 128, 1);
+    T.npass = 4; T.n = N_P; T.K = 128; T.R = nullptr; T.C = P + 384; T.ldc = 512; T.relu = 1;
+    madd(ms, T);
+    k_gm<<<gs.off[gs.nt] + ms.off[ms.nt], 256, 0, stream>>>(gs, ms);
+  }
+
+  {
+    MSup ms; ms.nt = 0;
     {
-      MTask& T = ma.t[0];
+      MTask T;
       mkpass(T, 0, DR + 128, 384, Wss_t + (size_t)0 * 16384, 128, nullptr, 0);
       mkpass(T, 1, ag9, 128, Wns_t + (size_t)0 * 16384, 128, b_s + 0 * 128, 1);
       mkpass(T, 2, DR + 128, 384, Wss_t + (size_t)1 * 16384, 128, nullptr, 0);
@@ -893,35 +951,39 @@
       mkpass(T, 4, DR + 128, 384, Wss_t + (size_t)6 * 16384, 128, nullptr, 0);
       mkpass(T, 5, ag15, 128, Wns_t + (size_t)6 * 16384, 128, b_s + 6 * 128, 1);
       T.npass = 6; T.n = N_DR; T.K = 128; T.R = nullptr; T.C = DR + 256; T.ldc = 384; T.relu = 1;
+      madd(ms, T);
     }
     {
-      MTask& T = ma.t[1];
+      MTask T;
       mkpass(T, 0, P + 128, 512, Wss_t + (size_t)2 * 16384, 128, nullptr, 0);
       mkpass(T, 1, ag11, 128, Wns_t + (size_t)2 * 16384, 128, b_s + 2 * 128, 1);
       mkpass(T, 2, P + 128, 512, Wss_t + (size_t)7 * 16384, 128, nullptr, 0);
       mkpass(T, 3, ag16, 128, Wns_t + (size_t)7 * 16384, 128, b_s + 7 * 128, 1);
       T.npass = 4; T.n = N_P; T.K = 128; T.R = nullptr; T.C = P + 256; T.ldc = 512; T.relu = 1;
-    }
-    k_mg<<<dim3((N_P + 63) / 64, 2), 256, 0, stream>>>(ma);
-  }
-
-  {
-    MArgs ma;
+      madd(ms, T);
+    }
+    k_gm<<<ms.off[ms.nt], 256, 0, stream>>>(g0, ms);
+  }
+
+  {
+    MSup ms; ms.nt = 0;
     for (int half = 0; half < 2; ++half) {
       {
-        MTask& T = ma.t[half];
+        MTask T;
         mkpass(T, 0, DR, 384, W1_t + (size_t)(half * 128) * 896, 896, pp[46] + half * 128, 1);
         T.npass = 1; T.n = N_DR; T.K = 384; T.R = nullptr;
         T.C = U_dr + half * 128; T.ldc = 256; T.relu = 0;
+        madd(ms, T);
       }
       {
-        MTask& T = ma.t[2 + half];
+        MTask T;
         mkpass(T, 0, P, 512, W1_t + (size_t)(half * 128) * 896 + 384, 896, nullptr, 1);
         T.npass = 1; T.n = N_P; T.K = 512; T.R = nullptr;
         T.C = U_p + half * 128; T.ldc = 256; T.relu = 0;
-      }
-    }
-    k_mg<<<dim3((N_P + 63) / 64, 4), 256, 0, stream>>>(ma);
+        madd(ms, T);
+      }
+    }
+    k_gm<<<ms.off[ms.nt], 256, 0, stream>>>(g0, ms);
   }
 
   k_hstat<<<256, 256, 0, stream>>>(x_dr, x_p, U_dr, U_p, st1, B);
```

Measured after the change: 1.282 ms. 1.05x slower.
